# Kernel tuning notes

Hardware: AMD Instinct MI355X
Metric: run time of the kernel (lower is better)

## Reference

```python
import jax, jax.numpy as jnp
import numpy as np

B, N, D, K = 2, 8192, 512, 16


def setup_inputs() -> dict:
    key = jax.random.key(0)
    k1, k2, k3, k4 = jax.random.split(key, 4)
    x = jax.random.normal(k1, (B, N, D), dtype=jnp.float32)
    xyz = jax.random.normal(k2, (B, N, 3), dtype=jnp.float32)
    # nn.Linear(d_model, 3*d_model): weight [3D, D], bias [3D]
    W_qkv = jax.random.normal(k3, (3 * D, D), dtype=jnp.float32) * 0.02
    b_qkv = jnp.zeros((3 * D,), dtype=jnp.float32)
    # nn.Linear(d_model, d_model)
    W_fc = jax.random.normal(k4, (D, D), dtype=jnp.float32) * 0.02
    b_fc = jnp.zeros((D,), dtype=jnp.float32)
    return {"x": x, "xyz": xyz, "W_qkv": W_qkv, "b_qkv": b_qkv, "W_fc": W_fc, "b_fc": b_fc}


def _knn_idx(xyz):
    # squared-distance KNN (same ordering as cdist): |a|^2 + |b|^2 - 2 a.b
    sq = jnp.sum(xyz * xyz, axis=-1)                      # [B, N]
    d2 = sq[:, :, None] + sq[:, None, :] - 2.0 * jnp.einsum('bnc,bmc->bnm', xyz, xyz)
    return jax.lax.top_k(-d2, K)[1]                       # [B, N, K] smallest distances


def reference(x, xyz, W_qkv, b_qkv, W_fc, b_fc):
    knn_idx = _knn_idx(xyz)                               # no-grad in original
    qkv = jnp.einsum('bnd,ed->bne', x, W_qkv) + b_qkv     # [B, N, 3D]
    qkv = qkv.reshape(B, N, 3, D)
    q, k, v = qkv[:, :, 0], qkv[:, :, 1], qkv[:, :, 2]    # [B, N, D]
    gather = jax.vmap(lambda arr, idx: arr[idx])          # per-batch neighbor gather
    k_neigh = gather(k, knn_idx)                          # [B, N, K, D]
    v_neigh = gather(v, knn_idx)                          # [B, N, K, D]
    # faithful to einsum('bnd,bnsk->bns', q, k_neigh): sums d and feature dims independently
    attn = (q.sum(-1)[:, :, None] * k_neigh.sum(-1)) / jnp.sqrt(jnp.float32(D))  # [B, N, K]
    attn = jax.nn.softmax(attn, axis=2)[..., None]        # [B, N, K, 1]
    x_out = (attn * v_neigh).sum(axis=2)                  # [B, N, D]
    return jnp.einsum('bnd,ed->bne', x_out, W_fc) + b_fc + x
```

## Files before the change

### kernel.cpp

```cpp
#include <hip/hip_runtime.h>

typedef _Float16 half_t;
typedef _Float16 half8 __attribute__((ext_vector_type(8)));
typedef _Float16 half4v __attribute__((ext_vector_type(4)));
typedef float f32x4 __attribute__((ext_vector_type(4)));
typedef float f32x2 __attribute__((ext_vector_type(2)));

#define NB 2
#define NN 8192
#define ND 512
#define NKNN 16
#define BN (NB*NN)

#define OFF_XH   0ull
#define OFF_VH   (OFF_XH  + (size_t)BN*ND*2)
#define OFF_XOH  (OFF_VH  + (size_t)BN*ND*2)
#define OFF_WVH  (OFF_XOH + (size_t)BN*ND*2)
#define OFF_WFCH (OFF_WVH + (size_t)ND*ND*2)
#define OFF_XW   (OFF_WFCH+ (size_t)ND*ND*2)
#define OFF_XW2  (OFF_XW  + (size_t)BN*16)
#define OFF_IDX  (OFF_XW2 + (size_t)BN*16)
#define OFF_WQC  (OFF_IDX + (size_t)BN*NKNN*4)
#define OFF_WKC  (OFF_WQC + 2048)
#define OFF_QKB  (OFF_WKC + 2048)
#define OFF_QS   (OFF_QKB + 256)
#define OFF_KS   (OFF_QS  + (size_t)BN*4)

__global__ __launch_bounds__(256) void kcolsum(const float* __restrict__ W,
                                               float* __restrict__ wq,
                                               float* __restrict__ wk) {
  int h = blockIdx.x >> 3, g = blockIdx.x & 7;
  int t = threadIdx.x, dl = t & 63, s = t >> 6;
  const float* Wb = W + (size_t)h * 512 * 512;
  int d = g * 64 + dl;
  float acc = 0.f;
  for (int e = s * 128; e < s * 128 + 128; ++e) acc += Wb[(size_t)e * 512 + d];
  __shared__ float red[4][64];
  red[s][dl] = acc;
  __syncthreads();
  if (s == 0) (h ? wk : wq)[d] = red[0][dl] + red[1][dl] + red[2][dl] + red[3][dl];
}

__global__ __launch_bounds__(512) void kbias(const float* __restrict__ b,
                                             float* __restrict__ qkb) {
  __shared__ float r0[512], r1[512];
  int t = threadIdx.x;
  r0[t] = b[t]; r1[t] = b[512 + t];
  __syncthreads();
  for (int s = 256; s; s >>= 1) {
    if (t < s) { r0[t] += r0[t + s]; r1[t] += r1[t + s]; }
    __syncthreads();
  }
  if (t == 0) { qkb[0] = r0[0]; qkb[1] = r1[0]; }
}

__global__ __launch_bounds__(256) void kconvw(const float* __restrict__ wqkv,
                                              const float* __restrict__ wfc,
                                              half_t* __restrict__ wvh,
                                              half_t* __restrict__ wfch) {
  int i = blockIdx.x * 256 + threadIdx.x;
  float4 a = ((const float4*)(wqkv + 1024 * 512))[i];
  half4v ha; ha[0]=(half_t)a.x; ha[1]=(half_t)a.y; ha[2]=(half_t)a.z; ha[3]=(half_t)a.w;
  *(half4v*)(wvh + (size_t)i * 4) = ha;
  float4 c = ((const float4*)wfc)[i];
  half4v hc; hc[0]=(half_t)c.x; hc[1]=(half_t)c.y; hc[2]=(half_t)c.z; hc[3]=(half_t)c.w;
  *(half4v*)(wfch + (size_t)i * 4) = hc;
}

__global__ __launch_bounds__(256) void kxh(const float* __restrict__ x,
                                           const float* __restrict__ wq,
                                           const float* __restrict__ wk,
                                           const float* __restrict__ qkb,
                                           half_t* __restrict__ xh,
                                           float* __restrict__ qs,
                                           float* __restrict__ ks) {
  int wid = blockIdx.x * 4 + (threadIdx.x >> 6);
  int l = threadIdx.x & 63;
  size_t base = (size_t)wid * ND + l * 8;
  float4 a0 = *(const float4*)(x + base);
  float4 a1 = *(const float4*)(x + base + 4);
  half8 h;
  h[0]=(half_t)a0.x; h[1]=(half_t)a0.y; h[2]=(half_t)a0.z; h[3]=(half_t)a0.w;
  h[4]=(half_t)a1.x; h[5]=(half_t)a1.y; h[6]=(half_t)a1.z; h[7]=(half_t)a1.w;
  *(half8*)(xh + base) = h;
  float4 q0 = ((const float4*)(wq + l * 8))[0], q1 = ((const float4*)(wq + l * 8))[1];
  float4 k0 = ((const float4*)(wk + l * 8))[0], k1 = ((const float4*)(wk + l * 8))[1];
  float dq = a0.x*q0.x + a0.y*q0.y + a0.z*q0.z + a0.w*q0.w
           + a1.x*q1.x + a1.y*q1.y + a1.z*q1.z + a1.w*q1.w;
  float dk = a0.x*k0.x + a0.y*k0.y + a0.z*k0.z + a0.w*k0.w
           + a1.x*k1.x + a1.y*k1.y + a1.z*k1.z + a1.w*k1.w;
  #pragma unroll
  for (int o = 32; o; o >>= 1) { dq += __shfl_xor(dq, o); dk += __shfl_xor(dk, o); }
  if (l == 0) { qs[wid] = dq + qkb[0]; ks[wid] = dk + qkb[1]; }
}

__global__ __launch_bounds__(256) void kxyzw(const float* __restrict__ xyz,
                                             float4* __restrict__ xw,
                                             float4* __restrict__ xw2) {
  int p = blockIdx.x * 256 + threadIdx.x;
  int b = p >> 12;
  int pl = p & 4095;
  int i0 = b * NN + pl * 2;
  const float* s = xyz + (size_t)i0 * 3;
  float x0 = s[0], y0 = s[1], z0 = s[2];
  float x1 = s[3], y1 = s[4], z1 = s[5];
  float sq0 = __fadd_rn(__fadd_rn(__fmul_rn(x0, x0), __fmul_rn(y0, y0)), __fmul_rn(z0, z0));
  float sq1 = __fadd_rn(__fadd_rn(__fmul_rn(x1, x1), __fmul_rn(y1, y1)), __fmul_rn(z1, z1));
  xw[i0]     = make_float4(x0, y0, z0, sq0);
  xw[i0 + 1] = make_float4(x1, y1, z1, sq1);
  xw2[(size_t)b * NN + pl]          = make_float4(x0, x1, y0, y1);
  xw2[(size_t)b * NN + NN/2 + pl]   = make_float4(z0, z1, sq0, sq1);
}

#define QPW 4
__global__ __launch_bounds__(256, 4) void kknn(const float4* __restrict__ xw,
                                               const float4* __restrict__ xw2,
                                               int* __restrict__ idxo) {
  const int tid = threadIdx.x;
  const int l = tid & 63;
  const int w = tid >> 6;
  const int b = blockIdx.x >> 9;
  const int qbase = (blockIdx.x & 511) * (4 * QPW) + w * QPW;
  const float4* xb  = xw  + (size_t)b * NN;
  const float4* xa2 = xw2 + (size_t)b * NN;
  const float4* xb2 = xa2 + NN / 2;

  f32x2 qxx[QPW], qyy[QPW], qzz[QPW], qww[QPW];
  #pragma unroll
  for (int qi = 0; qi < QPW; ++qi) {
    float4 qp = xb[qbase + qi];
    qxx[qi] = (f32x2){qp.x, qp.x};
    qyy[qi] = (f32x2){qp.y, qp.y};
    qzz[qi] = (f32x2){qp.z, qp.z};
    qww[qi] = (f32x2){qp.w, qp.w};
  }
  const f32x2 m2 = (f32x2){-2.0f, -2.0f};

  float mind0[QPW], mind1[QPW]; int mini0[QPW], mini1[QPW];
  #pragma unroll
  for (int qi = 0; qi < QPW; ++qi) {
    mind0[qi] = __builtin_inff(); mini0[qi] = 0x7fffffff;
    mind1[qi] = __builtin_inff(); mini1[qi] = 0x7fffffff;
  }

  #pragma unroll 4
  for (int it = 0; it < 64; ++it) {
    int p = it * 64 + l;
    float4 A  = xa2[p];
    float4 Bv = xb2[p];
    f32x2 cx = (f32x2){A.x, A.y};
    f32x2 cy = (f32x2){A.z, A.w};
    f32x2 cz = (f32x2){Bv.x, Bv.y};
    f32x2 cw = (f32x2){Bv.z, Bv.w};
    int ci0 = p * 2;
    #pragma unroll
    for (int qi = 0; qi < QPW; ++qi) {
      f32x2 dot = __builtin_elementwise_fma(qzz[qi], cz,
                    __builtin_elementwise_fma(qyy[qi], cy, qxx[qi] * cx));
      f32x2 s2 = qww[qi] + cw;
      f32x2 d2 = __builtin_elementwise_fma(m2, dot, s2);
      if (d2.x < mind0[qi]) { mind0[qi] = d2.x; mini0[qi] = ci0; }
      if (d2.y < mind1[qi]) { mind1[qi] = d2.y; mini1[qi] = ci0 + 1; }
    }
  }

  float mind[QPW]; int mini[QPW];
  #pragma unroll
  for (int qi = 0; qi < QPW; ++qi) {
    bool take1 = (mind1[qi] < mind0[qi]) ||
                 (mind1[qi] == mind0[qi] && mini1[qi] < mini0[qi]);
    mind[qi] = take1 ? mind1[qi] : mind0[qi];
    mini[qi] = take1 ? mini1[qi] : mini0[qi];
  }

  float kd[QPW]; int ki[QPW]; float wst[QPW];
  #pragma unroll
  for (int qi = 0; qi < QPW; ++qi) {
    float d = mind[qi]; int ii = mini[qi];
    #pragma unroll
    for (int k = 2; k <= 64; k <<= 1) {
      #pragma unroll
      for (int j = k >> 1; j > 0; j >>= 1) {
        float od = __shfl_xor(d, j);
        int   oi = __shfl_xor(ii, j);
        bool up = ((l & k) == 0);
        bool lower_lane = ((l & j) == 0);
        bool oless = (od < d) || (od == d && oi < ii);
        bool take = (up == lower_lane) ? oless : !oless;
        if (take) { d = od; ii = oi; }
      }
    }
    kd[qi] = __shfl(d, l & 15);
    ki[qi] = __shfl(ii, l & 15);
    wst[qi] = __shfl(d, 15);
  }

  auto insert = [&](bool ok, float dv, int iv, int qi) {
    unsigned long long m = __ballot(ok);
    while (m) {
      int a = __builtin_ctzll(m);
      m &= m - 1;
      float dc = __shfl(dv, a);
      int ic = __shfl(iv, a);
      bool lower = (kd[qi] < dc) || (kd[qi] == dc && ki[qi] < ic);
      int r = __popcll(__ballot(lower) & 0xFFFFull);
      if (r < 16) {
        float pd = __shfl_up(kd[qi], 1, 16);
        int pi = __shfl_up(ki[qi], 1, 16);
        int pp = l & 15;
        if (pp == r)      { kd[qi] = dc; ki[qi] = ic; }
        else if (pp > r)  { kd[qi] = pd; ki[qi] = pi; }
        wst[qi] = __shfl(kd[qi], 15, 16);
      }
    }
  };

  #pragma unroll 2
  for (int it = 0; it < 64; ++it) {
    int p = it * 64 + l;
    float4 A  = xa2[p];
    float4 Bv = xb2[p];
    f32x2 cx = (f32x2){A.x, A.y};
    f32x2 cy = (f32x2){A.z, A.w};
    f32x2 cz = (f32x2){Bv.x, Bv.y};
    f32x2 cw = (f32x2){Bv.z, Bv.w};
    int ci0 = p * 2;
    #pragma unroll
    for (int qi = 0; qi < QPW; ++qi) {
      f32x2 dot = __builtin_elementwise_fma(qzz[qi], cz,
                    __builtin_elementwise_fma(qyy[qi], cy, qxx[qi] * cx));
      f32x2 s2 = qww[qi] + cw;
      f32x2 d2 = __builtin_elementwise_fma(m2, dot, s2);
      bool ok0 = (d2.x <= wst[qi]) && (ci0 != mini[qi]);
      bool ok1 = (d2.y <= wst[qi]) && (ci0 + 1 != mini[qi]);
      insert(ok0, d2.x, ci0, qi);
      insert(ok1, d2.y, ci0 + 1, qi);
    }
  }

  if (l < 16) {
    #pragma unroll
    for (int qi = 0; qi < QPW; ++qi)
      idxo[((size_t)b * NN + qbase + qi) * NKNN + l] = ki[qi];
  }
}

__device__ __forceinline__ void gload16(const void* g, void* l) {
  __builtin_amdgcn_global_load_lds((const __attribute__((address_space(1))) void*)g,
                                   (__attribute__((address_space(3))) void*)l, 16, 0, 0);
}

template <int EPI>
__global__ __launch_bounds__(256) void kgemm(const half_t* __restrict__ A,
                                             const half_t* __restrict__ Bw,
                                             const float* __restrict__ bias,
                                             const float* __restrict__ resid,
                                             void* __restrict__ Cout) {
  __shared__ __align__(16) half_t As[128 * 64];
  __shared__ __align__(16) half_t Bs[128 * 64];
  const int tid = threadIdx.x;
  const int l = tid & 63;
  const int w = tid >> 6;
  const int wm = w >> 1, wn = w & 1;
  const int mt = blockIdx.x >> 2;
  const int nt = blockIdx.x & 3;
  const int lr = l & 15, lg = l >> 4;

  f32x4 acc[4][4];
  #pragma unroll
  for (int i = 0; i < 4; ++i)
    #pragma unroll
    for (int j = 0; j < 4; ++j) acc[i][j] = (f32x4){0.f, 0.f, 0.f, 0.f};

  for (int kt = 0; kt < 8; ++kt) {
    #pragma unroll
    for (int i = 0; i < 4; ++i) {
      int id = i * 256 + tid;
      int rr = id >> 3, cc = id & 7;
      gload16(A + (size_t)(mt * 128 + rr) * ND + kt * 64 + cc * 8,
              (void*)(As + (size_t)(i * 256 + w * 64) * 8));
      gload16(Bw + (size_t)(nt * 128 + rr) * ND + kt * 64 + cc * 8,
              (void*)(Bs + (size_t)(i * 256 + w * 64) * 8));
    }
    __syncthreads();
    #pragma unroll
    for (int kk = 0; kk < 2; ++kk) {
      half8 af[4], bf[4];
      #pragma unroll
      for (int mi = 0; mi < 4; ++mi)
        af[mi] = *(const half8*)(As + (wm * 64 + mi * 16 + lr) * 64 + kk * 32 + lg * 8);
      #pragma unroll
      for (int ni = 0; ni < 4; ++ni)
        bf[ni] = *(const half8*)(Bs + (wn * 64 + ni * 16 + lr) * 64 + kk * 32 + lg * 8);
      #pragma unroll
      for (int mi = 0; mi < 4; ++mi)
        #pragma unroll
        for (int ni = 0; ni < 4; ++ni)
          acc[mi][ni] = __builtin_amdgcn_mfma_f32_16x16x32_f16(af[mi], bf[ni], acc[mi][ni], 0, 0, 0);
    }
    __syncthreads();
  }

  #pragma unroll
  for (int mi = 0; mi < 4; ++mi) {
    #pragma unroll
    for (int ni = 0; ni < 4; ++ni) {
      int col = nt * 128 + wn * 64 + ni * 16 + lr;
      #pragma unroll
      for (int r4 = 0; r4 < 4; ++r4) {
        size_t row = (size_t)mt * 128 + wm * 64 + mi * 16 + lg * 4 + r4;
        float v = acc[mi][ni][r4] + bias[col];
        if (EPI == 0) ((half_t*)Cout)[row * ND + col] = (half_t)v;
        else          ((float*)Cout)[row * ND + col] = v + resid[row * ND + col];
      }
    }
  }
}

__global__ __launch_bounds__(256) void kattn(const int* __restrict__ idx,
                                             const float* __restrict__ qs,
                                             const float* __restrict__ ks,
                                             const half_t* __restrict__ vh,
                                             half_t* __restrict__ xoh) {
  int wid = blockIdx.x * 4 + (threadIdx.x >> 6);
  int l = threadIdx.x & 63;
  int b = wid >> 13;
  int j = l & 15;
  int nb = idx[(size_t)wid * NKNN + j];
  float ksv = ks[(size_t)b * NN + nb];
  float logit = __fdiv_rn(__fmul_rn(qs[wid], ksv), 22.627416997969522f);
  float mx = logit;
  #pragma unroll
  for (int o = 8; o; o >>= 1) mx = fmaxf(mx, __shfl_xor(mx, o, 16));
  float e = expf(logit - mx);
  float s = e;
  #pragma unroll
  for (int o = 8; o; o >>= 1) s += __shfl_xor(s, o, 16);
  float p = e / s;

  float acc[8] = {0.f, 0.f, 0.f, 0.f, 0.f, 0.f, 0.f, 0.f};
  #pragma unroll
  for (int t16 = 0; t16 < 16; ++t16) {
    float wj = __shfl(p, t16, 16);
    int ij = __shfl(nb, t16, 16);
    const half8 vv = *(const half8*)(vh + ((size_t)b * NN + ij) * ND + l * 8);
    #pragma unroll
    for (int u = 0; u < 8; ++u) acc[u] += wj * (float)vv[u];
  }
  half8 ho;
  #pragma unroll
  for (int u = 0; u < 8; ++u) ho[u] = (half_t)acc[u];
  *(half8*)(xoh + (size_t)wid * ND + l * 8) = ho;
}

extern "C" void kernel_launch(void* const* d_in, const int* in_sizes, int n_in,
                              void* d_out, int out_size, void* d_ws, size_t ws_size,
                              hipStream_t stream) {
  const float* x    = (const float*)d_in[0];
  const float* xyz  = (const float*)d_in[1];
  const float* wqkv = (const float*)d_in[2];
  const float* bqkv = (const float*)d_in[3];
  const float* wfc  = (const float*)d_in[4];
  const float* bfc  = (const float*)d_in[5];
  char* ws = (char*)d_ws;
  half_t* xh   = (half_t*)(ws + OFF_XH);
  half_t* vh   = (half_t*)(ws + OFF_VH);
  half_t* xoh  = (half_t*)(ws + OFF_XOH);
  half_t* wvh  = (half_t*)(ws + OFF_WVH);
  half_t* wfch = (half_t*)(ws + OFF_WFCH);
  float4* xw   = (float4*)(ws + OFF_XW);
  float4* xw2  = (float4*)(ws + OFF_XW2);
  int*    idx  = (int*)(ws + OFF_IDX);
  float*  wqc  = (float*)(ws + OFF_WQC);
  float*  wkc  = (float*)(ws + OFF_WKC);
  float*  qkb  = (float*)(ws + OFF_QKB);
  float*  qs   = (float*)(ws + OFF_QS);
  float*  ks   = (float*)(ws + OFF_KS);

  kcolsum<<<dim3(16),  dim3(256), 0, stream>>>(wqkv, wqc, wkc);
  kbias  <<<dim3(1),   dim3(512), 0, stream>>>(bqkv, qkb);
  kconvw <<<dim3(256), dim3(256), 0, stream>>>(wqkv, wfc, wvh, wfch);
  kxyzw  <<<dim3(32),  dim3(256), 0, stream>>>(xyz, xw, xw2);
  kxh    <<<dim3(4096),dim3(256), 0, stream>>>(x, wqc, wkc, qkb, xh, qs, ks);
  kknn   <<<dim3(1024),dim3(256), 0, stream>>>(xw, xw2, idx);
  kgemm<0><<<dim3(512),dim3(256), 0, stream>>>(xh, wvh, bqkv + 1024, (const float*)nullptr, (void*)vh);
  kattn  <<<dim3(4096),dim3(256), 0, stream>>>(idx, qs, ks, vh, xoh);
  kgemm<1><<<dim3(512),dim3(256), 0, stream>>>(xoh, wfch, bfc, x, d_out);
}
```

Baseline: 172.5 us.

## Stage KNN candidate tiles through double-buffered LDS with async global-to-LDS loads

The KNN kernel's two candidate sweeps now copy 512-point tiles of the packed coordinates into shared memory with global_load_lds, double-buffered so the next tile loads while the current one is processed. Previously each wave read candidates straight from global memory (L2 hits shared across the block's four waves). The aim is to cut redundant global/L2 traffic and hide load latency. It adds 32 KB of LDS per block and block-wide barriers per tile, which may reduce occupancy under the 4-blocks launch bound. There is no explicit wait on the async loads before the barrier, so correctness depends on the compiler inserting vmcnt waits.

New measurement: 173.6 us. No clear change (+0.7%).

```diff
diff --git a/kernel.cpp b/kernel.cpp
--- a/kernel.cpp
+++ b/kernel.cpp
@@ -112,10 +112,18 @@
   xw2[(size_t)b * NN + NN/2 + pl]   = make_float4(z0, z1, sq0, sq1);
 }
 
+__device__ __forceinline__ void gload16(const void* g, void* l) {
+  __builtin_amdgcn_global_load_lds((const __attribute__((address_space(1))) void*)g,
+                                   (__attribute__((address_space(3))) void*)l, 16, 0, 0);
+}
+
 #define QPW 4
+#define KTILE 512
 __global__ __launch_bounds__(256, 4) void kknn(const float4* __restrict__ xw,
                                                const float4* __restrict__ xw2,
                                                int* __restrict__ idxo) {
+  __shared__ __align__(16) float4 ldsA[2][KTILE];
+  __shared__ __align__(16) float4 ldsB[2][KTILE];
   const int tid = threadIdx.x;
   const int l = tid & 63;
   const int w = tid >> 6;
@@ -125,6 +133,14 @@
   const float4* xa2 = xw2 + (size_t)b * NN;
   const float4* xb2 = xa2 + NN / 2;
 
+  auto stage = [&](int t, int bi) {
+    int ts = t * KTILE;
+    gload16(xa2 + ts + w * 64 + l,        (void*)&ldsA[bi][w * 64]);
+    gload16(xa2 + ts + 256 + w * 64 + l,  (void*)&ldsA[bi][256 + w * 64]);
+    gload16(xb2 + ts + w * 64 + l,        (void*)&ldsB[bi][w * 64]);
+    gload16(xb2 + ts + 256 + w * 64 + l,  (void*)&ldsB[bi][256 + w * 64]);
+  };
+
   f32x2 qxx[QPW], qyy[QPW], qzz[QPW], qww[QPW];
   #pragma unroll
   for (int qi = 0; qi < QPW; ++qi) {
@@ -143,16 +159,12 @@
     mind1[qi] = __builtin_inff(); mini1[qi] = 0x7fffffff;
   }
 
-  #pragma unroll 4
-  for (int it = 0; it < 64; ++it) {
-    int p = it * 64 + l;
-    float4 A  = xa2[p];
-    float4 Bv = xb2[p];
+  auto body1 = [&](const float4& A, const float4& Bv, int pg) {
     f32x2 cx = (f32x2){A.x, A.y};
     f32x2 cy = (f32x2){A.z, A.w};
     f32x2 cz = (f32x2){Bv.x, Bv.y};
     f32x2 cw = (f32x2){Bv.z, Bv.w};
-    int ci0 = p * 2;
+    int ci0 = pg * 2;
     #pragma unroll
     for (int qi = 0; qi < QPW; ++qi) {
       f32x2 dot = __builtin_elementwise_fma(qzz[qi], cz,
@@ -162,6 +174,21 @@
       if (d2.x < mind0[qi]) { mind0[qi] = d2.x; mini0[qi] = ci0; }
       if (d2.y < mind1[qi]) { mind1[qi] = d2.y; mini1[qi] = ci0 + 1; }
     }
+  };
+
+  stage(0, 0);
+  __syncthreads();
+  #pragma unroll 2
+  for (int t = 0; t < 8; ++t) {
+    if (t < 7) stage(t + 1, (t + 1) & 1);
+    #pragma unroll
+    for (int it = 0; it < 8; ++it) {
+      int p = it * 64 + l;
+      float4 A  = ldsA[t & 1][p];
+      float4 Bv = ldsB[t & 1][p];
+      body1(A, Bv, t * KTILE + p);
+    }
+    __syncthreads();
   }
 
   float mind[QPW]; int mini[QPW];
@@ -215,16 +242,12 @@
     }
   };
 
-  #pragma unroll 2
-  for (int it = 0; it < 64; ++it) {
-    int p = it * 64 + l;
-    float4 A  = xa2[p];
-    float4 Bv = xb2[p];
+  auto body2 = [&](const float4& A, const float4& Bv, int pg) {
     f32x2 cx = (f32x2){A.x, A.y};
     f32x2 cy = (f32x2){A.z, A.w};
     f32x2 cz = (f32x2){Bv.x, Bv.y};
     f32x2 cw = (f32x2){Bv.z, Bv.w};
-    int ci0 = p * 2;
+    int ci0 = pg * 2;
     #pragma unroll
     for (int qi = 0; qi < QPW; ++qi) {
       f32x2 dot = __builtin_elementwise_fma(qzz[qi], cz,
@@ -236,6 +259,22 @@
       insert(ok0, d2.x, ci0, qi);
       insert(ok1, d2.y, ci0 + 1, qi);
     }
+  };
+
+  __syncthreads();
+  stage(0, 0);
+  __syncthreads();
+  #pragma unroll 2
+  for (int t = 0; t < 8; ++t) {
+    if (t < 7) stage(t + 1, (t + 1) & 1);
+    #pragma unroll
+    for (int it = 0; it < 8; ++it) {
+      int p = it * 64 + l;
+      float4 A  = ldsA[t & 1][p];
+      float4 Bv = ldsB[t & 1][p];
+      body2(A, Bv, t * KTILE + p);
+    }
+    __syncthreads();
   }
 
   if (l < 16) {
@@ -243,11 +282,6 @@
     for (int qi = 0; qi < QPW; ++qi)
       idxo[((size_t)b * NN + qbase + qi) * NKNN + l] = ki[qi];
   }
-}
-
-__device__ __forceinline__ void gload16(const void* g, void* l) {
-  __builtin_amdgcn_global_load_lds((const __attribute__((address_space(1))) void*)g,
-                                   (__attribute__((address_space(3))) void*)l, 16, 0, 0);
 }
 
 template <int EPI>
```
